# Kernel tuning notes

Hardware: AMD Instinct MI355X
Metric: run time of the kernel (lower is better)

The kernel has to match this reference:

```python
import jax, jax.numpy as jnp
import numpy as np

LMAX, MMAX = 4, 2
C = 128          # sphere_channels
MOUT = 128       # m_output_channels
N = 32768        # number of edges
K = sum(2 * min(l, MMAX) + 1 for l in range(LMAX + 1))  # 19 coefficients
LN_EPS = 1e-5


def build_to_m():
    # l-major ordering of (l, m) coefficients -> m-major permutation matrix
    ms = np.array([m for l in range(LMAX + 1)
                   for m in range(-min(l, MMAX), min(l, MMAX) + 1)])
    order = list(np.nonzero(ms == 0)[0])
    for m in range(1, MMAX + 1):
        order += list(np.nonzero(ms == m)[0]) + list(np.nonzero(ms == -m)[0])
    P = np.zeros((K, K), np.float32)
    P[np.arange(K), order] = 1.0
    return jnp.asarray(P)


TO_M = build_to_m()
M_SIZE = [LMAX + 1] + [LMAX - m + 1 for m in range(1, MMAX + 1)]  # [5, 4, 3]


def _layernorm(h, g, b):
    mu = jnp.mean(h, axis=-1, keepdims=True)
    var = jnp.mean(jnp.square(h - mu), axis=-1, keepdims=True)
    return (h - mu) * jax.lax.rsqrt(var + LN_EPS) * g + b


def _radial_mlp(x, w1, b1, g1, be1, w2, b2, g2, be2, w3, b3):
    h = jax.nn.silu(_layernorm(x @ w1.T + b1, g1, be1))
    h = jax.nn.silu(_layernorm(h @ w2.T + b2, g2, be2))
    return h @ w3.T + b3  # [N, 1536]


def setup_inputs() -> dict:
    key = jax.random.key(0)
    ks = jax.random.split(key, 16)
    s = 0.02
    return {
        "x": jax.random.normal(ks[0], (N, K, C), jnp.float32),
        "x_edge": jax.random.normal(ks[1], (N, C), jnp.float32),
        "fc0_w": jax.random.normal(ks[2], (MOUT * 5, 5 * C), jnp.float32) * s,
        "fc0_b": jax.random.normal(ks[3], (MOUT * 5,), jnp.float32) * s,
        "fc1_w": jax.random.normal(ks[4], (MOUT * 4, 4 * C), jnp.float32) * s,
        "fc2_w": jax.random.normal(ks[5], (MOUT * 3, 3 * C), jnp.float32) * s,
        "rad_w1": jax.random.normal(ks[6], (C, C), jnp.float32) * s,
        "rad_b1": jax.random.normal(ks[7], (C,), jnp.float32) * s,
        "rad_g1": jnp.ones((C,), jnp.float32),
        "rad_beta1": jnp.zeros((C,), jnp.float32),
        "rad_w2": jax.random.normal(ks[8], (C, C), jnp.float32) * s,
        "rad_b2": jax.random.normal(ks[9], (C,), jnp.float32) * s,
        "rad_g2": jnp.ones((C,), jnp.float32),
        "rad_beta2": jnp.zeros((C,), jnp.float32),
        "rad_w3": jax.random.normal(ks[10], (1536, C), jnp.float32) * s,
        "rad_b3": jax.random.normal(ks[11], (1536,), jnp.float32) * s,
    }


def reference(x, x_edge, fc0_w, fc0_b, fc1_w, fc2_w,
              rad_w1, rad_b1, rad_g1, rad_beta1,
              rad_w2, rad_b2, rad_g2, rad_beta2,
              rad_w3, rad_b3):
    n = x.shape[0]
    # reorder coefficients by m (to_m is a permutation)
    xm = jnp.einsum('nac,ba->nbc', x, TO_M)
    rad = _radial_mlp(x_edge, rad_w1, rad_b1, rad_g1, rad_beta1,
                      rad_w2, rad_b2, rad_g2, rad_beta2, rad_w3, rad_b3)

    # m = 0 block
    sz0 = M_SIZE[0]
    x0 = xm[:, :sz0].reshape(n, sz0 * C) * rad[:, :sz0 * C]
    y0 = (x0 @ fc0_w.T + fc0_b).reshape(n, sz0, MOUT)
    outs = [y0]

    offset, offr = sz0, sz0 * C
    for m, fcw in zip((1, 2), (fc1_w, fc2_w)):
        sz = M_SIZE[m]
        din = sz * C
        xb = xm[:, offset:offset + 2 * sz].reshape(n, 2, din)
        xb = xb * rad[:, offr:offr + din][:, None, :]  # FiLM radial scale
        yb = (xb @ fcw.T).reshape(n, 2 * sz, MOUT)
        outs.append(yb)
        offset += 2 * sz
        offr += din

    out = jnp.concatenate(outs, axis=1)  # [N, K, MOUT]
    # project back from m-major ordering
    return jnp.einsum('nac,ab->nbc', out, TO_M)
```

## Files before the change

### kernel.cpp

```cpp
#include <hip/hip_runtime.h>

typedef __bf16 bf16x8 __attribute__((ext_vector_type(8)));
typedef __bf16 bf16x4 __attribute__((ext_vector_type(4)));
typedef float f32x4 __attribute__((ext_vector_type(4)));

#define MFMA_16x16x32_BF16(a, b, c) __builtin_amdgcn_mfma_f32_16x16x32_bf16(a, b, c, 0, 0, 0)

typedef const __attribute__((address_space(1))) unsigned int* gas_ptr;
typedef __attribute__((address_space(3))) unsigned int* las_ptr;

__device__ __forceinline__ void gload_lds16(const void* g, void* l) {
    __builtin_amdgcn_global_load_lds((gas_ptr)(unsigned long long)g,
                                     (las_ptr)(unsigned long long)l, 16, 0, 0);
}

__constant__ int ORDER_C[19] = {0, 2, 6, 11, 16, 3, 7, 12, 17, 1, 5, 10, 15, 8, 13, 18, 4, 9, 14};

__global__ __launch_bounds__(256) void wxconv_kernel(
    const float* __restrict__ fc0, const float* __restrict__ fc1,
    const float* __restrict__ fc2, const float* __restrict__ rw1,
    const float* __restrict__ rw2, const float* __restrict__ rw3,
    const float* __restrict__ xe, __bf16* __restrict__ wo,
    __bf16* __restrict__ xo) {
    const int bid = blockIdx.x;
    const float* s;
    __bf16* o;
    int i4, rel;
    if (bid < 1024) {
        i4 = (bid * 256 + threadIdx.x) * 4;
        o = wo;
        if (i4 < 409600)      { s = fc0; rel = i4; }
        else if (i4 < 671744) { s = fc1; rel = i4 - 409600; }
        else if (i4 < 819200) { s = fc2; rel = i4 - 671744; }
        else if (i4 < 835584) { s = rw1; rel = i4 - 819200; }
        else if (i4 < 851968) { s = rw2; rel = i4 - 835584; }
        else                  { s = rw3; rel = i4 - 851968; }
    } else {
        i4 = ((bid - 1024) * 256 + threadIdx.x) * 4;
        o = xo; s = xe; rel = i4;
    }
    float4 v = *(const float4*)(s + rel);
    bf16x4 b;
    b[0] = (__bf16)v.x; b[1] = (__bf16)v.y; b[2] = (__bf16)v.z; b[3] = (__bf16)v.w;
    *(bf16x4*)(o + i4) = b;
}

__global__ __launch_bounds__(256) void gemmln_kernel(
    const __bf16* __restrict__ Ain, const __bf16* __restrict__ Wb,
    const float* __restrict__ bvec, const float* __restrict__ gv,
    const float* __restrict__ bev, __bf16* __restrict__ hs) {
    __shared__ __align__(16) char smem[65536];
    __bf16* As = (__bf16*)smem;
    __bf16* Bs = (__bf16*)(smem + 32768);
    float*  Fs = (float*)smem;
    const int tid = threadIdx.x;
    const int w = tid >> 6, lane = tid & 63;
    const int quad = lane >> 4, l16 = lane & 15;
    const int e0 = blockIdx.x * 128;

    {
        const char* ga = (const char*)(Ain + (size_t)e0 * 128);
        const char* gb = (const char*)Wb;
        for (int r = 0; r < 8; ++r) {
            int boff = (r * 4 + w) * 1024 + lane * 16;
            int soff = boff ^ (((boff >> 8) & 15) << 4);
            gload_lds16(ga + soff, (char*)As + boff);
            gload_lds16(gb + soff, (char*)Bs + boff);
        }
    }
    __syncthreads();

    const int wr = w >> 1, wc = w & 1;
    f32x4 acc[4][4] = {};
    for (int ks = 0; ks < 4; ++ks) {
        bf16x8 af[4], bfr[4];
        for (int i = 0; i < 4; ++i) {
            int ar = wr * 64 + i * 16 + l16;
            af[i] = *(const bf16x8*)&As[ar * 128 + ((ks * 32 + quad * 8) ^ ((ar & 15) << 3))];
        }
        for (int j = 0; j < 4; ++j) {
            int br = wc * 64 + j * 16 + l16;
            bfr[j] = *(const bf16x8*)&Bs[br * 128 + ((ks * 32 + quad * 8) ^ ((br & 15) << 3))];
        }
        for (int i = 0; i < 4; ++i)
            for (int j = 0; j < 4; ++j)
                acc[i][j] = MFMA_16x16x32_BF16(af[i], bfr[j], acc[i][j]);
    }
    __syncthreads();

    float bc[4];
    for (int j = 0; j < 4; ++j) bc[j] = bvec[wc * 64 + j * 16 + l16];
    for (int i = 0; i < 4; ++i)
        for (int j = 0; j < 4; ++j)
            for (int r = 0; r < 4; ++r)
                Fs[(wr * 64 + i * 16 + quad * 4 + r) * 128 + wc * 64 + j * 16 + l16] =
                    acc[i][j][r] + bc[j];
    __syncthreads();

    const float gl = gv[lane], gh = gv[lane + 64];
    const float bl = bev[lane], bh = bev[lane + 64];
    for (int it = 0; it < 32; ++it) {
        const int row = it * 4 + w;
        float a = Fs[row * 128 + lane];
        float b = Fs[row * 128 + lane + 64];
        float s = a + b;
        s += __shfl_xor(s, 1);  s += __shfl_xor(s, 2);  s += __shfl_xor(s, 4);
        s += __shfl_xor(s, 8);  s += __shfl_xor(s, 16); s += __shfl_xor(s, 32);
        const float mu = s * (1.f / 128.f);
        const float da = a - mu, db = b - mu;
        float v = da * da + db * db;
        v += __shfl_xor(v, 1);  v += __shfl_xor(v, 2);  v += __shfl_xor(v, 4);
        v += __shfl_xor(v, 8);  v += __shfl_xor(v, 16); v += __shfl_xor(v, 32);
        const float rs = rsqrtf(v * (1.f / 128.f) + 1e-5f);
        float ya = da * rs * gl + bl;
        float yb = db * rs * gh + bh;
        ya = ya / (1.f + __expf(-ya));
        yb = yb / (1.f + __expf(-yb));
        hs[(size_t)(e0 + row) * 128 + lane] = (__bf16)ya;
        hs[(size_t)(e0 + row) * 128 + lane + 64] = (__bf16)yb;
    }
}

__global__ __launch_bounds__(256) void radial3_film_kernel(
    const __bf16* __restrict__ h2g, const __bf16* __restrict__ w3b,
    const float* __restrict__ b3, const float* __restrict__ xg,
    __bf16* __restrict__ Aws) {
    __shared__ __align__(16) __bf16 As[128 * 128];
    __shared__ __align__(16) __bf16 Bs[128 * 128];
    const int tid = threadIdx.x;
    const int w = tid >> 6, lane = tid & 63;
    const int quad = lane >> 4, l16 = lane & 15;
    const int y = blockIdx.y;
    const int e0 = blockIdx.x * 128, n0 = y * 128;

    {
        const char* ga = (const char*)(h2g + (size_t)e0 * 128);
        const char* gb = (const char*)(w3b + (size_t)n0 * 128);
        for (int r = 0; r < 8; ++r) {
            int boff = (r * 4 + w) * 1024 + lane * 16;
            int soff = boff ^ (((boff >> 8) & 15) << 4);
            gload_lds16(ga + soff, (char*)As + boff);
            gload_lds16(gb + soff, (char*)Bs + boff);
        }
    }
    __syncthreads();

    const int wr = w >> 1, wc = w & 1;
    f32x4 acc[4][4] = {};
    for (int ks = 0; ks < 4; ++ks) {
        bf16x8 af[4], bfr[4];
        for (int i = 0; i < 4; ++i) {
            int ar = wr * 64 + i * 16 + l16;
            af[i] = *(const bf16x8*)&As[ar * 128 + ((ks * 32 + quad * 8) ^ ((ar & 15) << 3))];
        }
        for (int j = 0; j < 4; ++j) {
            int br = wc * 64 + j * 16 + l16;
            bfr[j] = *(const bf16x8*)&Bs[br * 128 + ((ks * 32 + quad * 8) ^ ((br & 15) << 3))];
        }
        for (int i = 0; i < 4; ++i)
            for (int j = 0; j < 4; ++j)
                acc[i][j] = MFMA_16x16x32_BF16(af[i], bfr[j], acc[i][j]);
    }
    __syncthreads();

    float bcol[4];
    for (int j = 0; j < 4; ++j) bcol[j] = b3[n0 + wc * 64 + j * 16 + l16];
    for (int i = 0; i < 4; ++i)
        for (int j = 0; j < 4; ++j)
            for (int r = 0; r < 4; ++r) {
                int row = wr * 64 + i * 16 + quad * 4 + r;
                int col = wc * 64 + j * 16 + l16;
                As[row * 128 + col] = (__bf16)(acc[i][j][r] + bcol[j]);
            }
    __syncthreads();

    int nb, bs0, bs1;
    if (y < 5)      { nb = 1; bs0 = y;     bs1 = 0; }
    else if (y < 9) { nb = 2; bs0 = y;     bs1 = y + 4; }
    else            { nb = 2; bs0 = y + 4; bs1 = y + 7; }

    for (int t = 0; t < nb; ++t) {
        const int b = t ? bs1 : bs0;
        const int xrow = ORDER_C[b];
        for (int r = 0; r < 8; ++r) {
            int idx = r * 256 + tid;
            int e = idx >> 4, c = (idx & 15) * 8;
            bf16x8 rv = *(const bf16x8*)&As[e * 128 + c];
            const float* xp = xg + (size_t)(e0 + e) * 2432 + xrow * 128 + c;
            float4 x0 = *(const float4*)xp;
            float4 x1 = *(const float4*)(xp + 4);
            bf16x8 av;
            av[0] = (__bf16)(x0.x * (float)rv[0]);
            av[1] = (__bf16)(x0.y * (float)rv[1]);
            av[2] = (__bf16)(x0.z * (float)rv[2]);
            av[3] = (__bf16)(x0.w * (float)rv[3]);
            av[4] = (__bf16)(x1.x * (float)rv[4]);
            av[5] = (__bf16)(x1.y * (float)rv[5]);
            av[6] = (__bf16)(x1.z * (float)rv[6]);
            av[7] = (__bf16)(x1.w * (float)rv[7]);
            *(bf16x8*)(Aws + (size_t)(e0 + e) * 2432 + b * 128 + c) = av;
        }
    }
}

__global__ __launch_bounds__(256) void so2_gemm_kernel(
    const __bf16* __restrict__ Aws, const __bf16* __restrict__ wfc0,
    const __bf16* __restrict__ wfc1, const __bf16* __restrict__ wfc2,
    const float* __restrict__ fc0b, float* __restrict__ outg) {
    __shared__ __align__(16) __bf16 As[2][128 * 64];
    __shared__ __align__(16) __bf16 Bs[2][128 * 64];
    const int tid = threadIdx.x;
    const int w = tid >> 6, lane = tid & 63;
    const int quad = lane >> 4, l16 = lane & 15;
    const int e0 = blockIdx.x * 128;
    const int y = blockIdx.y;

    int bstart, sz;
    const __bf16* W;
    if (y < 5)       { bstart = 0;  sz = 5; W = wfc0; }
    else if (y < 9)  { bstart = 5;  sz = 4; W = wfc1; }
    else if (y < 13) { bstart = 9;  sz = 4; W = wfc1; }
    else if (y < 16) { bstart = 13; sz = 3; W = wfc2; }
    else             { bstart = 16; sz = 3; W = wfc2; }
    const int K = sz * 128, s_out = y - bstart, nkt = 2 * sz;
    const char* abase = (const char*)Aws + (size_t)bstart * 256;
    const char* wbase = (const char*)W + (size_t)s_out * 128 * K * 2;

#define STAGE(buf, kt)                                                             \
    {                                                                              \
        const char* ak = abase + (size_t)(kt) * 128;                               \
        const char* wk = wbase + (size_t)(kt) * 128;                               \
        for (int r = 0; r < 4; ++r) {                                              \
            int boff = (r * 4 + w) * 1024 + lane * 16;                             \
            int row = boff >> 7, kb = boff & 127;                                  \
            int skb = kb ^ ((row & 7) << 4);                                       \
            gload_lds16(ak + (size_t)(e0 + row) * 4864 + skb, (char*)As[buf] + boff); \
            gload_lds16(wk + (size_t)row * (size_t)(K * 2) + skb, (char*)Bs[buf] + boff); \
        }                                                                          \
    }

    const int wr = w >> 1, wc = w & 1;
    f32x4 acc[4][4] = {};
    STAGE(0, 0);
    __syncthreads();
    for (int kt = 0; kt < nkt; ++kt) {
        const int cur = kt & 1;
        if (kt + 1 < nkt) STAGE(cur ^ 1, kt + 1);
        for (int ks = 0; ks < 2; ++ks) {
            bf16x8 af[4], bfr[4];
            for (int i = 0; i < 4; ++i) {
                int ar = wr * 64 + i * 16 + l16;
                af[i] = *(const bf16x8*)&As[cur][ar * 64 + ((ks * 32 + quad * 8) ^ ((ar & 7) << 3))];
            }
            for (int j = 0; j < 4; ++j) {
                int br = wc * 64 + j * 16 + l16;
                bfr[j] = *(const bf16x8*)&Bs[cur][br * 64 + ((ks * 32 + quad * 8) ^ ((br & 7) << 3))];
            }
            for (int i = 0; i < 4; ++i)
                for (int j = 0; j < 4; ++j)
                    acc[i][j] = MFMA_16x16x32_BF16(af[i], bfr[j], acc[i][j]);
        }
        __syncthreads();
    }
#undef STAGE

    const int outrow = ORDER_C[y];
    float bv[4];
    for (int j = 0; j < 4; ++j)
        bv[j] = (y < 5) ? fc0b[s_out * 128 + wc * 64 + j * 16 + l16] : 0.f;
    for (int i = 0; i < 4; ++i)
        for (int j = 0; j < 4; ++j) {
            const int col = wc * 64 + j * 16 + l16;
            for (int r = 0; r < 4; ++r) {
                const int row = e0 + wr * 64 + i * 16 + quad * 4 + r;
                outg[(size_t)row * 2432 + outrow * 128 + col] = acc[i][j][r] + bv[j];
            }
        }
}

extern "C" void kernel_launch(void* const* d_in, const int* in_sizes, int n_in,
                              void* d_out, int out_size, void* d_ws, size_t ws_size,
                              hipStream_t stream) {
    const float* x       = (const float*)d_in[0];
    const float* x_edge  = (const float*)d_in[1];
    const float* fc0_w   = (const float*)d_in[2];
    const float* fc0_b   = (const float*)d_in[3];
    const float* fc1_w   = (const float*)d_in[4];
    const float* fc2_w   = (const float*)d_in[5];
    const float* rad_w1  = (const float*)d_in[6];
    const float* rad_b1  = (const float*)d_in[7];
    const float* rad_g1  = (const float*)d_in[8];
    const float* rad_be1 = (const float*)d_in[9];
    const float* rad_w2  = (const float*)d_in[10];
    const float* rad_b2  = (const float*)d_in[11];
    const float* rad_g2  = (const float*)d_in[12];
    const float* rad_be2 = (const float*)d_in[13];
    const float* rad_w3  = (const float*)d_in[14];
    const float* rad_b3  = (const float*)d_in[15];
    float* out = (float*)d_out;

    const int N = in_sizes[0] / (19 * 128);

    __bf16* wb  = (__bf16*)d_ws;
    __bf16* sh  = (__bf16*)((char*)d_ws + (2u << 20));
    __bf16* Aws = (__bf16*)((char*)d_ws + (10u << 20));
    __bf16* h1  = Aws;
    __bf16* wfc0 = wb;
    __bf16* wfc1 = wb + 409600;
    __bf16* wfc2 = wb + 671744;
    __bf16* w1b  = wb + 819200;
    __bf16* w2b  = wb + 835584;
    __bf16* w3b  = wb + 851968;

    wxconv_kernel<<<dim3(5120), dim3(256), 0, stream>>>(fc0_w, fc1_w, fc2_w, rad_w1,
                                                        rad_w2, rad_w3, x_edge, wb, sh);
    gemmln_kernel<<<dim3(N / 128), dim3(256), 0, stream>>>(sh, w1b, rad_b1, rad_g1,
                                                           rad_be1, h1);
    gemmln_kernel<<<dim3(N / 128), dim3(256), 0, stream>>>(h1, w2b, rad_b2, rad_g2,
                                                           rad_be2, sh);
    radial3_film_kernel<<<dim3(N / 128, 12), dim3(256), 0, stream>>>(sh, w3b, rad_b3,
                                                                     x, Aws);
    so2_gemm_kernel<<<dim3(N / 128, 19), dim3(256), 0, stream>>>(Aws, wfc0, wfc1, wfc2,
                                                                 fc0_b, out);
}
```

Before: 760.7 us.

## Halve gemmln tile, remap so2 grid, split load/compute barriers, stage output via LDS

The gemmln kernel now handles 64 edges per block instead of 128, which lowers its LDS use and doubles its block count. The so2 GEMM moves to a 1D grid with a swizzled block-to-tile mapping and adds a two-block occupancy hint. Its main loop now uses explicit vmcnt waits and raw barriers, loads all LDS fragments before raising priority for the MFMA burst, and writes the epilogue through LDS as coalesced float4 stores. The grid constant 8*608 only matches N=32768 (608 = 4864/8), so the kernel assumes that edge count.

```diff
diff --git a/kernel.cpp b/kernel.cpp
--- a/kernel.cpp
+++ b/kernel.cpp
@@ -49,40 +49,44 @@
     const __bf16* __restrict__ Ain, const __bf16* __restrict__ Wb,
     const float* __restrict__ bvec, const float* __restrict__ gv,
     const float* __restrict__ bev, __bf16* __restrict__ hs) {
-    __shared__ __align__(16) char smem[65536];
+    __shared__ __align__(16) char smem[49152];
     __bf16* As = (__bf16*)smem;
-    __bf16* Bs = (__bf16*)(smem + 32768);
+    __bf16* Bs = (__bf16*)(smem + 16384);
     float*  Fs = (float*)smem;
     const int tid = threadIdx.x;
     const int w = tid >> 6, lane = tid & 63;
     const int quad = lane >> 4, l16 = lane & 15;
-    const int e0 = blockIdx.x * 128;
+    const int e0 = blockIdx.x * 64;
 
     {
         const char* ga = (const char*)(Ain + (size_t)e0 * 128);
         const char* gb = (const char*)Wb;
+        for (int r = 0; r < 4; ++r) {
+            int boff = (r * 4 + w) * 1024 + lane * 16;
+            int soff = boff ^ (((boff >> 8) & 15) << 4);
+            gload_lds16(ga + soff, (char*)As + boff);
+        }
         for (int r = 0; r < 8; ++r) {
             int boff = (r * 4 + w) * 1024 + lane * 16;
             int soff = boff ^ (((boff >> 8) & 15) << 4);
-            gload_lds16(ga + soff, (char*)As + boff);
             gload_lds16(gb + soff, (char*)Bs + boff);
         }
     }
     __syncthreads();
 
     const int wr = w >> 1, wc = w & 1;
-    f32x4 acc[4][4] = {};
+    f32x4 acc[2][4] = {};
     for (int ks = 0; ks < 4; ++ks) {
-        bf16x8 af[4], bfr[4];
-        for (int i = 0; i < 4; ++i) {
-            int ar = wr * 64 + i * 16 + l16;
+        bf16x8 af[2], bfr[4];
+        for (int i = 0; i < 2; ++i) {
+            int ar = wr * 32 + i * 16 + l16;
             af[i] = *(const bf16x8*)&As[ar * 128 + ((ks * 32 + quad * 8) ^ ((ar & 15) << 3))];
         }
         for (int j = 0; j < 4; ++j) {
             int br = wc * 64 + j * 16 + l16;
             bfr[j] = *(const bf16x8*)&Bs[br * 128 + ((ks * 32 + quad * 8) ^ ((br & 15) << 3))];
         }
-        for (int i = 0; i < 4; ++i)
+        for (int i = 0; i < 2; ++i)
             for (int j = 0; j < 4; ++j)
                 acc[i][j] = MFMA_16x16x32_BF16(af[i], bfr[j], acc[i][j]);
     }
@@ -90,16 +94,16 @@
 
     float bc[4];
     for (int j = 0; j < 4; ++j) bc[j] = bvec[wc * 64 + j * 16 + l16];
-    for (int i = 0; i < 4; ++i)
+    for (int i = 0; i < 2; ++i)
         for (int j = 0; j < 4; ++j)
             for (int r = 0; r < 4; ++r)
-                Fs[(wr * 64 + i * 16 + quad * 4 + r) * 128 + wc * 64 + j * 16 + l16] =
+                Fs[(wr * 32 + i * 16 + quad * 4 + r) * 128 + wc * 64 + j * 16 + l16] =
                     acc[i][j][r] + bc[j];
     __syncthreads();
 
     const float gl = gv[lane], gh = gv[lane + 64];
     const float bl = bev[lane], bh = bev[lane + 64];
-    for (int it = 0; it < 32; ++it) {
+    for (int it = 0; it < 16; ++it) {
         const int row = it * 4 + w;
         float a = Fs[row * 128 + lane];
         float b = Fs[row * 128 + lane + 64];
@@ -203,17 +207,19 @@
     }
 }
 
-__global__ __launch_bounds__(256) void so2_gemm_kernel(
+__global__ __launch_bounds__(256, 2) void so2_gemm_kernel(
     const __bf16* __restrict__ Aws, const __bf16* __restrict__ wfc0,
     const __bf16* __restrict__ wfc1, const __bf16* __restrict__ wfc2,
     const float* __restrict__ fc0b, float* __restrict__ outg) {
-    __shared__ __align__(16) __bf16 As[2][128 * 64];
-    __shared__ __align__(16) __bf16 Bs[2][128 * 64];
+    __shared__ __align__(16) char smem[65536];
     const int tid = threadIdx.x;
     const int w = tid >> 6, lane = tid & 63;
     const int quad = lane >> 4, l16 = lane & 15;
-    const int e0 = blockIdx.x * 128;
-    const int y = blockIdx.y;
+
+    const int bid = blockIdx.x;
+    const int wg = (bid & 7) * 608 + (bid >> 3);
+    const int y = wg % 19;
+    const int e0 = (wg / 19) * 128;
 
     int bstart, sz;
     const __bf16* W;
@@ -226,41 +232,56 @@
     const char* abase = (const char*)Aws + (size_t)bstart * 256;
     const char* wbase = (const char*)W + (size_t)s_out * 128 * K * 2;
 
-#define STAGE(buf, kt)                                                             \
-    {                                                                              \
-        const char* ak = abase + (size_t)(kt) * 128;                               \
-        const char* wk = wbase + (size_t)(kt) * 128;                               \
-        for (int r = 0; r < 4; ++r) {                                              \
-            int boff = (r * 4 + w) * 1024 + lane * 16;                             \
-            int row = boff >> 7, kb = boff & 127;                                  \
-            int skb = kb ^ ((row & 7) << 4);                                       \
-            gload_lds16(ak + (size_t)(e0 + row) * 4864 + skb, (char*)As[buf] + boff); \
-            gload_lds16(wk + (size_t)row * (size_t)(K * 2) + skb, (char*)Bs[buf] + boff); \
-        }                                                                          \
+#define STAGE(buf, kt)                                                              \
+    {                                                                               \
+        const char* ak = abase + (size_t)(kt) * 128;                                \
+        const char* wk = wbase + (size_t)(kt) * 128;                                \
+        char* la = smem + (buf) * 16384;                                            \
+        char* lb = smem + 32768 + (buf) * 16384;                                    \
+        for (int r = 0; r < 4; ++r) {                                               \
+            int boff = (r * 4 + w) * 1024 + lane * 16;                              \
+            int row = boff >> 7, kb = boff & 127;                                   \
+            int skb = kb ^ ((row & 7) << 4);                                        \
+            gload_lds16(ak + (size_t)(e0 + row) * 4864 + skb, la + boff);           \
+            gload_lds16(wk + (size_t)row * (size_t)(K * 2) + skb, lb + boff);       \
+        }                                                                           \
     }
 
     const int wr = w >> 1, wc = w & 1;
     f32x4 acc[4][4] = {};
     STAGE(0, 0);
-    __syncthreads();
     for (int kt = 0; kt < nkt; ++kt) {
         const int cur = kt & 1;
-        if (kt + 1 < nkt) STAGE(cur ^ 1, kt + 1);
+        if (kt + 1 < nkt) {
+            STAGE(cur ^ 1, kt + 1);
+            asm volatile("s_waitcnt vmcnt(8)" ::: "memory");
+        } else {
+            asm volatile("s_waitcnt vmcnt(0)" ::: "memory");
+        }
+        __builtin_amdgcn_s_barrier();
+
+        const __bf16* Asc = (const __bf16*)(smem + cur * 16384);
+        const __bf16* Bsc = (const __bf16*)(smem + 32768 + cur * 16384);
+        bf16x8 af[2][4], bfr[2][4];
         for (int ks = 0; ks < 2; ++ks) {
-            bf16x8 af[4], bfr[4];
             for (int i = 0; i < 4; ++i) {
                 int ar = wr * 64 + i * 16 + l16;
-                af[i] = *(const bf16x8*)&As[cur][ar * 64 + ((ks * 32 + quad * 8) ^ ((ar & 7) << 3))];
+                af[ks][i] = *(const bf16x8*)&Asc[ar * 64 + ((ks * 32 + quad * 8) ^ ((ar & 7) << 3))];
             }
             for (int j = 0; j < 4; ++j) {
                 int br = wc * 64 + j * 16 + l16;
-                bfr[j] = *(const bf16x8*)&Bs[cur][br * 64 + ((ks * 32 + quad * 8) ^ ((br & 7) << 3))];
+                bfr[ks][j] = *(const bf16x8*)&Bsc[br * 64 + ((ks * 32 + quad * 8) ^ ((br & 7) << 3))];
             }
+        }
+        asm volatile("s_waitcnt lgkmcnt(0)" ::: "memory");
+        __builtin_amdgcn_s_barrier();
+
+        __builtin_amdgcn_s_setprio(1);
+        for (int ks = 0; ks < 2; ++ks)
             for (int i = 0; i < 4; ++i)
                 for (int j = 0; j < 4; ++j)
-                    acc[i][j] = MFMA_16x16x32_BF16(af[i], bfr[j], acc[i][j]);
-        }
-        __syncthreads();
+                    acc[i][j] = MFMA_16x16x32_BF16(af[ks][i], bfr[ks][j], acc[i][j]);
+        __builtin_amdgcn_s_setprio(0);
     }
 #undef STAGE
 
@@ -268,14 +289,19 @@
     float bv[4];
     for (int j = 0; j < 4; ++j)
         bv[j] = (y < 5) ? fc0b[s_out * 128 + wc * 64 + j * 16 + l16] : 0.f;
+    float* Fs = (float*)smem;
     for (int i = 0; i < 4; ++i)
-        for (int j = 0; j < 4; ++j) {
-            const int col = wc * 64 + j * 16 + l16;
-            for (int r = 0; r < 4; ++r) {
-                const int row = e0 + wr * 64 + i * 16 + quad * 4 + r;
-                outg[(size_t)row * 2432 + outrow * 128 + col] = acc[i][j][r] + bv[j];
-            }
-        }
+        for (int j = 0; j < 4; ++j)
+            for (int r = 0; r < 4; ++r)
+                Fs[(wr * 64 + i * 16 + quad * 4 + r) * 128 + wc * 64 + j * 16 + l16] =
+                    acc[i][j][r] + bv[j];
+    __syncthreads();
+    for (int t = 0; t < 16; ++t) {
+        int idx = t * 256 + tid;
+        int row = idx >> 5, c4 = (idx & 31) * 4;
+        *(float4*)(outg + (size_t)(e0 + row) * 2432 + outrow * 128 + c4) =
+            *(const float4*)&Fs[row * 128 + c4];
+    }
 }
 
 extern "C" void kernel_launch(void* const* d_in, const int* in_sizes, int n_in,
@@ -314,12 +340,12 @@
 
     wxconv_kernel<<<dim3(5120), dim3(256), 0, stream>>>(fc0_w, fc1_w, fc2_w, rad_w1,
                                                         rad_w2, rad_w3, x_edge, wb, sh);
-    gemmln_kernel<<<dim3(N / 128), dim3(256), 0, stream>>>(sh, w1b, rad_b1, rad_g1,
-                                                           rad_be1, h1);
-    gemmln_kernel<<<dim3(N / 128), dim3(256), 0, stream>>>(h1, w2b, rad_b2, rad_g2,
-                                                           rad_be2, sh);
+    gemmln_kernel<<<dim3(N / 64), dim3(256), 0, stream>>>(sh, w1b, rad_b1, rad_g1,
+                                                          rad_be1, h1);
+    gemmln_kernel<<<dim3(N / 64), dim3(256), 0, stream>>>(h1, w2b, rad_b2, rad_g2,
+                                                          rad_be2, sh);
     radial3_film_kernel<<<dim3(N / 128, 12), dim3(256), 0, stream>>>(sh, w3b, rad_b3,
                                                                      x, Aws);
-    so2_gemm_kernel<<<dim3(N / 128, 19), dim3(256), 0, stream>>>(Aws, wfc0, wfc1, wfc2,
-                                                                 fc0_b, out);
-}
+    so2_gemm_kernel<<<dim3(8 * 608), dim3(256), 0, stream>>>(Aws, wfc0, wfc1, wfc2,
+                                                             fc0_b, out);
+}
```

Measured after the change: 725.1 us. 1.05x faster.
